# Performance work log

Hardware: AMD Instinct MI355X
Metric: run time of the kernel (lower is better)

## Reference

```python
import jax, jax.numpy as jnp
import numpy as np

# Static conv hyperparameters (match init_kwargs / setup_inputs)
PAD = 1
DIL = 1
STRIDE_VAL = 2.5          # continuous stride value used in setup_inputs
INT_STRIDE = 2            # floor(STRIDE_VAL): used for output-size arithmetic (static)


def _bilinear_take(x, pos, axis):
    """Linearly interpolate x along `axis` at fractional positions `pos`.

    pos has shape [O, K]; the sampled axis of x is replaced by the two axes
    (O, K). Out-of-range samples contribute zero (deform-conv convention).
    """
    n = x.shape[axis]
    p0 = jnp.floor(pos).astype(jnp.int32)
    frac = (pos - p0.astype(pos.dtype))
    out_shape = x.shape[:axis] + pos.shape + x.shape[axis + 1:]
    bshape = (1,) * axis + pos.shape + (1,) * (x.ndim - axis - 1)

    def take(p):
        valid = ((p >= 0) & (p < n)).astype(x.dtype).reshape(bshape)
        v = jnp.take(x, jnp.clip(p, 0, n - 1).reshape(-1), axis=axis)
        return v.reshape(out_shape) * valid

    w = frac.reshape(bshape).astype(x.dtype)
    return take(p0) * (1.0 - w) + take(p0 + 1) * w


def setup_inputs() -> dict:
    key = jax.random.key(0)
    k1, k2, k3 = jax.random.split(key, 3)
    x = jax.random.normal(k1, (32, 128, 64, 64), dtype=jnp.float32)
    weight = jax.random.normal(k2, (256, 128, 3, 3), dtype=jnp.float32) * 0.05
    bias = jax.random.normal(k3, (256,), dtype=jnp.float32)
    stride_h = jnp.full((1,), STRIDE_VAL, dtype=jnp.float32)
    stride_w = jnp.full((1,), STRIDE_VAL, dtype=jnp.float32)
    return {"x": x, "weight": weight, "bias": bias,
            "stride_h": stride_h, "stride_w": stride_w}


def reference(x, weight, bias, stride_h, stride_w):
    B, C, H, W = x.shape
    O, _, KH, KW = weight.shape
    # output size uses floor(stride), exactly as StrideConv2dFunction._output_size
    OH = (H + 2 * PAD - DIL * (KH - 1) - 1) // INT_STRIDE + 1
    OW = (W + 2 * PAD - DIL * (KW - 1) - 1) // INT_STRIDE + 1
    # fractional im2col sampling positions: out_idx * stride - pad + k * dilation
    pos_h = (jnp.arange(OH, dtype=jnp.float32)[:, None] * stride_h[0]
             - PAD + jnp.arange(KH, dtype=jnp.float32)[None, :] * DIL)  # [OH,KH]
    pos_w = (jnp.arange(OW, dtype=jnp.float32)[:, None] * stride_w[0]
             - PAD + jnp.arange(KW, dtype=jnp.float32)[None, :] * DIL)  # [OW,KW]
    rows = _bilinear_take(x, pos_h, axis=2)          # [B,C,OH,KH,W]
    patches = _bilinear_take(rows, pos_w, axis=4)    # [B,C,OH,KH,OW,KW]
    out = jnp.einsum('bcpkql,ockl->bopq', patches, weight)  # [B,O,OH,OW]
    return out + bias[None, :, None, None]
```

## Files before the change

### kernel.cpp

```cpp
#include <hip/hip_runtime.h>
#include <cstddef>

#define BB  32
#define CC  128
#define HH  64
#define WW  64
#define OO  256
#define OHH 32
#define OWW 32
#define YSTR 196
#define PSTR 296
#define ROWE (32 * YSTR)

typedef __bf16 bf16x8 __attribute__((ext_vector_type(8)));
typedef __bf16 bf16x4 __attribute__((ext_vector_type(4)));
typedef float  f32x4  __attribute__((ext_vector_type(4)));

__global__ void wtrans_bf16_kernel(const float* __restrict__ w, __bf16* __restrict__ wt) {
    int idx = blockIdx.x * 256 + threadIdx.x;
    if (idx >= OO * 9 * CC) return;
    int c    = idx & 127;
    int rest = idx >> 7;
    int k    = rest % 9;
    int o    = rest / 9;
    wt[idx] = (__bf16)w[((size_t)o * CC + c) * 9 + k];
}

__global__ __launch_bounds__(512, 2)
void conv_mfma_kernel(const float* __restrict__ x, const __bf16* __restrict__ wt,
                      const float* __restrict__ bias, const float* __restrict__ shp,
                      const float* __restrict__ swp, float* __restrict__ out) {
    __shared__ __align__(16) __bf16 yrbuf[4 + 4 * ROWE];
    __shared__ __align__(16) __bf16 pT[128 * PSTR];

    const int tid = threadIdx.x;
    const int b   = blockIdx.x;
    const int p0  = blockIdx.y * 4;
    const float sh = shp[0];
    const float sw = swp[0];

    float fh_[4];
    int   hb_[4];
    bool  oob[4];
#pragma unroll
    for (int pi = 0; pi < 4; ++pi) {
        float hpos = (float)(p0 + pi) * sh - 1.0f;
        float hbf  = floorf(hpos);
        fh_[pi] = hpos - hbf;
        hb_[pi] = (int)hbf;
        oob[pi] = (hb_[pi] >= HH || hb_[pi] <= -4);
    }

    if (oob[0] && oob[1] && oob[2] && oob[3]) {
#pragma unroll
        for (int j = 0; j < 16; ++j) {
            int fi = j * 512 + tid;
            int o  = fi >> 5;
            int rem = fi & 31;
            int pi = rem >> 3;
            int qf = rem & 7;
            float bv = bias[o];
            float4 r; r.x = bv; r.y = bv; r.z = bv; r.w = bv;
            *(float4*)(out + (((size_t)b * OO + o) * OHH + p0 + pi) * OWW + qf * 4) = r;
        }
        return;
    }

    const int piA = tid >> 7;
    const int t7  = tid & 127;
    const int cA  = t7 >> 2;
    const int cg0 = (t7 & 3) * 16;
    const float fhA = fh_[piA];
    int  hrA[4];
    bool rvA[4];
#pragma unroll
    for (int r = 0; r < 4; ++r) {
        hrA[r] = hb_[piA] + r;
        rvA[r] = (hrA[r] >= 0) && (hrA[r] < HH);
    }
    __bf16* yrA = yrbuf + 4 + piA * ROWE;

    const int piB = tid >> 7;
    const int qB  = (tid >> 2) & 31;
    const int cB  = (tid & 3) * 8;
    const float wposB = (float)qB * sw - 1.0f;
    const float wbfB  = floorf(wposB);
    const float fw    = wposB - wbfB;
    const int   wbq   = (int)wbfB;
    const int   wba   = min(wbq & ~3, 60);
    const int   e     = wbq - wba;
    const bool  g1 = e >= 1, g2 = e >= 2, g3 = e >= 3;
    bool mv[4];
#pragma unroll
    for (int j = 0; j < 4; ++j) mv[j] = ((unsigned)(wbq + j) < (unsigned)WW);
    const __bf16* yrB = yrbuf + 4 + piB * ROWE;
    __bf16* pqRow = pT + (piB * 32 + qB) * PSTR;

    const int wv = tid >> 6;
    const int l  = tid & 63;
    const int lr = l & 15;
    const int lg = l >> 4;
    const int o0 = wv * 32;

    f32x4 acc[2][8];
#pragma unroll
    for (int ot = 0; ot < 2; ++ot)
#pragma unroll
        for (int nt = 0; nt < 8; ++nt) acc[ot][nt] = (f32x4)0.0f;

    if (tid < 4) yrbuf[tid] = (__bf16)0.0f;

    for (int chunk = 0; chunk < 4; ++chunk) {
        const int c0 = chunk * 32;

        {
            const float* xp = x + ((size_t)(b * CC + c0 + cA) * HH) * WW;
            float4 v[4][4];
#pragma unroll
            for (int r = 0; r < 4; ++r) {
                if (rvA[r]) {
                    const float* rp = xp + (size_t)hrA[r] * WW + cg0;
#pragma unroll
                    for (int g = 0; g < 4; ++g) v[r][g] = *(const float4*)(rp + g * 4);
                } else {
#pragma unroll
                    for (int g = 0; g < 4; ++g) { v[r][g].x = 0.f; v[r][g].y = 0.f; v[r][g].z = 0.f; v[r][g].w = 0.f; }
                }
            }
            __bf16* yw = yrA + cA * YSTR + cg0;
#pragma unroll
            for (int kh = 0; kh < 3; ++kh) {
#pragma unroll
                for (int g = 0; g < 4; ++g) {
                    bf16x4 t;
                    t[0] = (__bf16)(v[kh][g].x + fhA * (v[kh + 1][g].x - v[kh][g].x));
                    t[1] = (__bf16)(v[kh][g].y + fhA * (v[kh + 1][g].y - v[kh][g].y));
                    t[2] = (__bf16)(v[kh][g].z + fhA * (v[kh + 1][g].z - v[kh][g].z));
                    t[3] = (__bf16)(v[kh][g].w + fhA * (v[kh + 1][g].w - v[kh][g].w));
                    *(bf16x4*)(yw + kh * 64 + g * 4) = t;
                }
            }
        }
        __syncthreads();

#pragma unroll
        for (int g = 0; g < 2; ++g) {
            const int cc0 = cB + g * 4;
            float tv[3][3][4];
#pragma unroll
            for (int ci = 0; ci < 4; ++ci) {
                const __bf16* yc = yrB + (cc0 + ci) * YSTR + wba;
#pragma unroll
                for (int kh = 0; kh < 3; ++kh) {
                    bf16x4 a  = *(const bf16x4*)(yc + kh * 64);
                    bf16x4 bq = *(const bf16x4*)(yc + kh * 64 + 4);
                    float v0 = (float)a[0], v1 = (float)a[1], v2 = (float)a[2], v3 = (float)a[3];
                    float v4 = (float)bq[0], v5 = (float)bq[1], v6 = (float)bq[2];
                    float s0 = g1 ? v1 : v0; s0 = g2 ? v2 : s0; s0 = g3 ? v3 : s0;
                    float s1 = g1 ? v2 : v1; s1 = g2 ? v3 : s1; s1 = g3 ? v4 : s1;
                    float s2 = g1 ? v3 : v2; s2 = g2 ? v4 : s2; s2 = g3 ? v5 : s2;
                    float s3 = g1 ? v4 : v3; s3 = g2 ? v5 : s3; s3 = g3 ? v6 : s3;
                    s0 = mv[0] ? s0 : 0.0f;
                    s1 = mv[1] ? s1 : 0.0f;
                    s2 = mv[2] ? s2 : 0.0f;
                    s3 = mv[3] ? s3 : 0.0f;
                    tv[kh][0][ci] = s0 + fw * (s1 - s0);
                    tv[kh][1][ci] = s1 + fw * (s2 - s1);
                    tv[kh][2][ci] = s2 + fw * (s3 - s2);
                }
            }
#pragma unroll
            for (int kh = 0; kh < 3; ++kh)
#pragma unroll
                for (int kw = 0; kw < 3; ++kw) {
                    bf16x4 pr;
                    pr[0] = (__bf16)tv[kh][kw][0];
                    pr[1] = (__bf16)tv[kh][kw][1];
                    pr[2] = (__bf16)tv[kh][kw][2];
                    pr[3] = (__bf16)tv[kh][kw][3];
                    *(bf16x4*)(pqRow + (kh * 3 + kw) * 32 + cc0) = pr;
                }
        }
        __syncthreads();

        __builtin_amdgcn_s_setprio(1);
#pragma unroll
        for (int k = 0; k < 9; ++k) {
            const __bf16* wp = wt + ((size_t)(o0 + lr) * 9 + k) * CC + c0 + lg * 8;
            bf16x8 a0 = *(const bf16x8*)(wp);
            bf16x8 a1 = *(const bf16x8*)(wp + (size_t)16 * 9 * CC);
            bf16x8 bfr[8];
#pragma unroll
            for (int nt = 0; nt < 8; ++nt)
                bfr[nt] = *(const bf16x8*)&pT[(nt * 16 + lr) * PSTR + k * 32 + lg * 8];
#pragma unroll
            for (int nt = 0; nt < 8; ++nt) {
                acc[0][nt] = __builtin_amdgcn_mfma_f32_16x16x32_bf16(a0, bfr[nt], acc[0][nt], 0, 0, 0);
                acc[1][nt] = __builtin_amdgcn_mfma_f32_16x16x32_bf16(a1, bfr[nt], acc[1][nt], 0, 0, 0);
            }
        }
        __builtin_amdgcn_s_setprio(0);
    }

#pragma unroll
    for (int ot = 0; ot < 2; ++ot) {
#pragma unroll
        for (int r = 0; r < 4; ++r) {
            int o = o0 + ot * 16 + lg * 4 + r;
            float bv = bias[o];
#pragma unroll
            for (int nt = 0; nt < 8; ++nt) {
                int pi = nt >> 1;
                int qc = (nt & 1) * 16 + lr;
                out[(((size_t)b * OO + o) * OHH + p0 + pi) * OWW + qc] = acc[ot][nt][r] + bv;
            }
        }
    }
}

__global__ __launch_bounds__(256)
void conv_fallback_kernel(const float* __restrict__ x, const float* __restrict__ w,
                          const float* __restrict__ bias, const float* __restrict__ shp,
                          const float* __restrict__ swp, float* __restrict__ out) {
    __shared__ __align__(16) float xr[4][WW];
    __shared__ __align__(16) float patch[9][OWW];
    const int tid = threadIdx.x;
    const int p = blockIdx.y;
    const int b = blockIdx.x;
    const float sh = shp[0];
    const float sw = swp[0];
    const float hpos = (float)p * sh - 1.0f;
    const float hbf  = floorf(hpos);
    const float fh   = hpos - hbf;
    const int   hb   = (int)hbf;
    const int og = tid & 63;
    const int qg = tid >> 6;
    const int o0 = og * 4;
    const int q0 = qg * 8;
    const int rr   = tid >> 6;
    const int colc = tid & 63;
    const int rowg = hb + rr;
    const bool rv = (rowg >= 0) && (rowg < HH);
    float acc[4][8];
#pragma unroll
    for (int i = 0; i < 4; ++i)
#pragma unroll
        for (int j = 0; j < 8; ++j) acc[i][j] = 0.0f;
    for (int c = 0; c < CC; ++c) {
        float vv = 0.0f;
        if (rv) vv = x[(((size_t)b * CC + c) * HH + rowg) * WW + colc];
        xr[rr][colc] = vv;
        __syncthreads();
        for (int it = tid; it < 9 * OWW; it += 256) {
            int k = it >> 5; int q = it & 31;
            int kh = k / 3;  int kw = k - kh * 3;
            float wpos = (float)q * sw - 1.0f + (float)kw;
            float wbf = floorf(wpos);
            float fw = wpos - wbf;
            int wb = (int)wbf;
            float x00 = 0, x01 = 0, x10 = 0, x11 = 0;
            if (wb >= 0 && wb < WW)         { x00 = xr[kh][wb];     x10 = xr[kh + 1][wb]; }
            if (wb + 1 >= 0 && wb + 1 < WW) { x01 = xr[kh][wb + 1]; x11 = xr[kh + 1][wb + 1]; }
            float top = x00 * (1.0f - fw) + x01 * fw;
            float bot = x10 * (1.0f - fw) + x11 * fw;
            patch[k][q] = top * (1.0f - fh) + bot * fh;
        }
        __syncthreads();
        const float4* pv = (const float4*)&patch[0][0];
#pragma unroll
        for (int k = 0; k < 9; ++k) {
            const float* wb_ = w + (size_t)o0 * (CC * 9) + c * 9 + k;
            float wvv[4] = {wb_[0], wb_[1 * CC * 9], wb_[2 * CC * 9], wb_[3 * CC * 9]};
            float4 pa = pv[k * 8 + (q0 >> 2)];
            float4 pb = pv[k * 8 + (q0 >> 2) + 1];
#pragma unroll
            for (int oo2 = 0; oo2 < 4; ++oo2) {
                acc[oo2][0] += wvv[oo2] * pa.x; acc[oo2][1] += wvv[oo2] * pa.y;
                acc[oo2][2] += wvv[oo2] * pa.z; acc[oo2][3] += wvv[oo2] * pa.w;
                acc[oo2][4] += wvv[oo2] * pb.x; acc[oo2][5] += wvv[oo2] * pb.y;
                acc[oo2][6] += wvv[oo2] * pb.z; acc[oo2][7] += wvv[oo2] * pb.w;
            }
        }
    }
    float4 bv = ((const float4*)bias)[og];
    float bvv[4] = {bv.x, bv.y, bv.z, bv.w};
#pragma unroll
    for (int oo2 = 0; oo2 < 4; ++oo2) {
        size_t off = (((size_t)b * OO + o0 + oo2) * OHH + p) * OWW + q0;
        float4 r0, r1;
        r0.x = acc[oo2][0] + bvv[oo2]; r0.y = acc[oo2][1] + bvv[oo2];
        r0.z = acc[oo2][2] + bvv[oo2]; r0.w = acc[oo2][3] + bvv[oo2];
        r1.x = acc[oo2][4] + bvv[oo2]; r1.y = acc[oo2][5] + bvv[oo2];
        r1.z = acc[oo2][6] + bvv[oo2]; r1.w = acc[oo2][7] + bvv[oo2];
        *(float4*)(out + off)     = r0;
        *(float4*)(out + off + 4) = r1;
    }
}

extern "C" void kernel_launch(void* const* d_in, const int* in_sizes, int n_in,
                              void* d_out, int out_size, void* d_ws, size_t ws_size,
                              hipStream_t stream) {
    const float* x    = (const float*)d_in[0];
    const float* w    = (const float*)d_in[1];
    const float* bias = (const float*)d_in[2];
    const float* shp  = (const float*)d_in[3];
    const float* swp  = (const float*)d_in[4];
    float* out = (float*)d_out;

    const size_t wt_bytes = (size_t)OO * 9 * CC * sizeof(__bf16);
    if (ws_size >= wt_bytes) {
        __bf16* wtp = (__bf16*)d_ws;
        int n = OO * 9 * CC;
        wtrans_bf16_kernel<<<(n + 255) / 256, 256, 0, stream>>>(w, wtp);
        dim3 grid(BB, OHH / 4);
        conv_mfma_kernel<<<grid, 512, 0, stream>>>(x, wtp, bias, shp, swp, out);
    } else {
        dim3 grid(BB, OHH);
        conv_fallback_kernel<<<grid, 256, 0, stream>>>(x, w, bias, shp, swp, out);
    }
}
```

Measured before the change: 55.08 us.

## Software-pipeline conv stages across half-tiles with double-buffered LDS and register-cached weights

The per-chunk loop is split into two half-tiles (row pairs), each with its own LDS buffers. Global loads for the next chunk, the horizontal interpolation of one half and the MFMA work on the other half are interleaved so loads and ALU overlap with matrix work across fewer barrier-separated phases. Weight fragments for a chunk are loaded once into registers and reused for both halves. The cost is higher register pressure (9x2 bf16x8 weight fragments plus pinned prefetch registers), which could cause spills or reduce occupancy at 512 threads with 2 blocks per CU.

```diff
diff --git a/kernel.cpp b/kernel.cpp
--- a/kernel.cpp
+++ b/kernel.cpp
@@ -9,8 +9,10 @@
 #define OHH 32
 #define OWW 32
 #define YSTR 196
+#define PROW (32 * YSTR)
+#define YRHALF (2 * PROW)
 #define PSTR 296
-#define ROWE (32 * YSTR)
+#define PTHALF (64 * PSTR)
 
 typedef __bf16 bf16x8 __attribute__((ext_vector_type(8)));
 typedef __bf16 bf16x4 __attribute__((ext_vector_type(4)));
@@ -30,8 +32,8 @@
 void conv_mfma_kernel(const float* __restrict__ x, const __bf16* __restrict__ wt,
                       const float* __restrict__ bias, const float* __restrict__ shp,
                       const float* __restrict__ swp, float* __restrict__ out) {
-    __shared__ __align__(16) __bf16 yrbuf[4 + 4 * ROWE];
-    __shared__ __align__(16) __bf16 pT[128 * PSTR];
+    __shared__ __align__(16) __bf16 yrbuf[8 + 2 * YRHALF + 8];
+    __shared__ __align__(16) __bf16 pT[2 * PTHALF];
 
     const int tid = threadIdx.x;
     const int b   = blockIdx.x;
@@ -66,23 +68,23 @@
         return;
     }
 
-    const int piA = tid >> 7;
-    const int t7  = tid & 127;
-    const int cA  = t7 >> 2;
-    const int cg0 = (t7 & 3) * 16;
-    const float fhA = fh_[piA];
-    int  hrA[4];
-    bool rvA[4];
-#pragma unroll
-    for (int r = 0; r < 4; ++r) {
-        hrA[r] = hb_[piA] + r;
-        rvA[r] = (hrA[r] >= 0) && (hrA[r] < HH);
-    }
-    __bf16* yrA = yrbuf + 4 + piA * ROWE;
-
-    const int piB = tid >> 7;
-    const int qB  = (tid >> 2) & 31;
-    const int cB  = (tid & 3) * 8;
+    const int pi2A = tid >> 8;
+    const int cA   = (tid >> 3) & 31;
+    const int colg = (tid & 7) * 8;
+    int  hr4[4][4];
+    bool rv4[4][4];
+#pragma unroll
+    for (int pi = 0; pi < 4; ++pi)
+#pragma unroll
+        for (int r = 0; r < 4; ++r) {
+            hr4[pi][r] = hb_[pi] + r;
+            rv4[pi][r] = (hr4[pi][r] >= 0) && (hr4[pi][r] < HH);
+        }
+
+    const int qB2  = tid >> 3;
+    const int pi2B = qB2 >> 5;
+    const int qB   = qB2 & 31;
+    const int cg0  = (tid & 7) * 4;
     const float wposB = (float)qB * sw - 1.0f;
     const float wbfB  = floorf(wposB);
     const float fw    = wposB - wbfB;
@@ -93,8 +95,6 @@
     bool mv[4];
 #pragma unroll
     for (int j = 0; j < 4; ++j) mv[j] = ((unsigned)(wbq + j) < (unsigned)WW);
-    const __bf16* yrB = yrbuf + 4 + piB * ROWE;
-    __bf16* pqRow = pT + (piB * 32 + qB) * PSTR;
 
     const int wv = tid >> 6;
     const int l  = tid & 63;
@@ -108,99 +108,140 @@
 #pragma unroll
         for (int nt = 0; nt < 8; ++nt) acc[ot][nt] = (f32x4)0.0f;
 
-    if (tid < 4) yrbuf[tid] = (__bf16)0.0f;
-
-    for (int chunk = 0; chunk < 4; ++chunk) {
-        const int c0 = chunk * 32;
-
-        {
-            const float* xp = x + ((size_t)(b * CC + c0 + cA) * HH) * WW;
-            float4 v[4][4];
-#pragma unroll
-            for (int r = 0; r < 4; ++r) {
-                if (rvA[r]) {
-                    const float* rp = xp + (size_t)hrA[r] * WW + cg0;
-#pragma unroll
-                    for (int g = 0; g < 4; ++g) v[r][g] = *(const float4*)(rp + g * 4);
-                } else {
-#pragma unroll
-                    for (int g = 0; g < 4; ++g) { v[r][g].x = 0.f; v[r][g].y = 0.f; v[r][g].z = 0.f; v[r][g].w = 0.f; }
-                }
-            }
-            __bf16* yw = yrA + cA * YSTR + cg0;
+    if (tid < 8) yrbuf[tid] = (__bf16)0.0f;
+
+    float4 vx[2][4];
+    bf16x8 wa[9][2];
+
+    auto aIssue = [&](int c0, int P) {
+        const int p = P * 2 + pi2A;
+        const float* xp = x + ((size_t)(b * CC + c0 + cA) * HH) * WW + colg;
+#pragma unroll
+        for (int r = 0; r < 4; ++r) {
+            float4 t0 = {0.f, 0.f, 0.f, 0.f}, t1 = t0;
+            if (rv4[p][r]) {
+                const float* rp = xp + (size_t)hr4[p][r] * WW;
+                t0 = *(const float4*)(rp);
+                t1 = *(const float4*)(rp + 4);
+            }
+            vx[0][r] = t0;
+            vx[1][r] = t1;
+        }
+    };
+
+    auto aFinish = [&](int P) {
+        const int p = P * 2 + pi2A;
+        const float fh = fh_[p];
+        __bf16* yw = yrbuf + 8 + P * YRHALF + pi2A * PROW + cA * YSTR + colg;
+#pragma unroll
+        for (int kh = 0; kh < 3; ++kh) {
+#pragma unroll
+            for (int h = 0; h < 2; ++h) {
+                float4 a = vx[h][kh], d = vx[h][kh + 1];
+                bf16x4 t;
+                t[0] = (__bf16)(a.x + fh * (d.x - a.x));
+                t[1] = (__bf16)(a.y + fh * (d.y - a.y));
+                t[2] = (__bf16)(a.z + fh * (d.z - a.z));
+                t[3] = (__bf16)(a.w + fh * (d.w - a.w));
+                *(bf16x4*)(yw + kh * 64 + h * 4) = t;
+            }
+        }
+    };
+
+    auto doB = [&](int P) {
+        const __bf16* ybase = yrbuf + 8 + P * YRHALF + pi2B * PROW;
+        __bf16* pq = pT + P * PTHALF + qB2 * PSTR;
+        float tv[3][3][4];
+#pragma unroll
+        for (int ci = 0; ci < 4; ++ci) {
+            const __bf16* yc = ybase + (cg0 + ci) * YSTR + wba;
 #pragma unroll
             for (int kh = 0; kh < 3; ++kh) {
-#pragma unroll
-                for (int g = 0; g < 4; ++g) {
-                    bf16x4 t;
-                    t[0] = (__bf16)(v[kh][g].x + fhA * (v[kh + 1][g].x - v[kh][g].x));
-                    t[1] = (__bf16)(v[kh][g].y + fhA * (v[kh + 1][g].y - v[kh][g].y));
-                    t[2] = (__bf16)(v[kh][g].z + fhA * (v[kh + 1][g].z - v[kh][g].z));
-                    t[3] = (__bf16)(v[kh][g].w + fhA * (v[kh + 1][g].w - v[kh][g].w));
-                    *(bf16x4*)(yw + kh * 64 + g * 4) = t;
-                }
-            }
-        }
+                bf16x4 a  = *(const bf16x4*)(yc + kh * 64);
+                bf16x4 bq = *(const bf16x4*)(yc + kh * 64 + 4);
+                float v0 = (float)a[0], v1 = (float)a[1], v2 = (float)a[2], v3 = (float)a[3];
+                float v4 = (float)bq[0], v5 = (float)bq[1], v6 = (float)bq[2];
+                float s0 = g1 ? v1 : v0; s0 = g2 ? v2 : s0; s0 = g3 ? v3 : s0;
+                float s1 = g1 ? v2 : v1; s1 = g2 ? v3 : s1; s1 = g3 ? v4 : s1;
+                float s2 = g1 ? v3 : v2; s2 = g2 ? v4 : s2; s2 = g3 ? v5 : s2;
+                float s3 = g1 ? v4 : v3; s3 = g2 ? v5 : s3; s3 = g3 ? v6 : s3;
+                s0 = mv[0] ? s0 : 0.0f;
+                s1 = mv[1] ? s1 : 0.0f;
+                s2 = mv[2] ? s2 : 0.0f;
+                s3 = mv[3] ? s3 : 0.0f;
+                tv[kh][0][ci] = s0 + fw * (s1 - s0);
+                tv[kh][1][ci] = s1 + fw * (s2 - s1);
+                tv[kh][2][ci] = s2 + fw * (s3 - s2);
+            }
+        }
+#pragma unroll
+        for (int kh = 0; kh < 3; ++kh)
+#pragma unroll
+            for (int kw = 0; kw < 3; ++kw) {
+                bf16x4 pr;
+                pr[0] = (__bf16)tv[kh][kw][0];
+                pr[1] = (__bf16)tv[kh][kw][1];
+                pr[2] = (__bf16)tv[kh][kw][2];
+                pr[3] = (__bf16)tv[kh][kw][3];
+                *(bf16x4*)(pq + (kh * 3 + kw) * 32 + cg0) = pr;
+            }
+    };
+
+    auto doM = [&](int c0, int nh, bool loadA) {
+        __builtin_amdgcn_s_setprio(1);
+#pragma unroll
+        for (int k = 0; k < 9; ++k) {
+            if (loadA) {
+                const __bf16* wp = wt + ((size_t)(o0 + lr) * 9 + k) * CC + c0 + lg * 8;
+                wa[k][0] = *(const bf16x8*)(wp);
+                wa[k][1] = *(const bf16x8*)(wp + (size_t)16 * 9 * CC);
+            }
+            const __bf16* pb = pT + nh * PTHALF + lr * PSTR + k * 32 + lg * 8;
+            bf16x8 b0 = *(const bf16x8*)(pb);
+            bf16x8 b1 = *(const bf16x8*)(pb + 16 * PSTR);
+            bf16x8 b2 = *(const bf16x8*)(pb + 32 * PSTR);
+            bf16x8 b3 = *(const bf16x8*)(pb + 48 * PSTR);
+            acc[0][nh * 4 + 0] = __builtin_amdgcn_mfma_f32_16x16x32_bf16(wa[k][0], b0, acc[0][nh * 4 + 0], 0, 0, 0);
+            acc[0][nh * 4 + 1] = __builtin_amdgcn_mfma_f32_16x16x32_bf16(wa[k][0], b1, acc[0][nh * 4 + 1], 0, 0, 0);
+            acc[0][nh * 4 + 2] = __builtin_amdgcn_mfma_f32_16x16x32_bf16(wa[k][0], b2, acc[0][nh * 4 + 2], 0, 0, 0);
+            acc[0][nh * 4 + 3] = __builtin_amdgcn_mfma_f32_16x16x32_bf16(wa[k][0], b3, acc[0][nh * 4 + 3], 0, 0, 0);
+            acc[1][nh * 4 + 0] = __builtin_amdgcn_mfma_f32_16x16x32_bf16(wa[k][1], b0, acc[1][nh * 4 + 0], 0, 0, 0);
+            acc[1][nh * 4 + 1] = __builtin_amdgcn_mfma_f32_16x16x32_bf16(wa[k][1], b1, acc[1][nh * 4 + 1], 0, 0, 0);
+            acc[1][nh * 4 + 2] = __builtin_amdgcn_mfma_f32_16x16x32_bf16(wa[k][1], b2, acc[1][nh * 4 + 2], 0, 0, 0);
+            acc[1][nh * 4 + 3] = __builtin_amdgcn_mfma_f32_16x16x32_bf16(wa[k][1], b3, acc[1][nh * 4 + 3], 0, 0, 0);
+        }
+        __builtin_amdgcn_s_setprio(0);
+    };
+
+#define PIN_VX() asm volatile("" :: \
+    "v"(vx[0][0].x), "v"(vx[0][1].x), "v"(vx[0][2].x), "v"(vx[0][3].x), \
+    "v"(vx[1][0].x), "v"(vx[1][1].x), "v"(vx[1][2].x), "v"(vx[1][3].x))
+
+    aIssue(0, 0); aFinish(0);
+    __syncthreads();
+    aIssue(0, 1); doB(0); aFinish(1);
+    __syncthreads();
+
+#pragma unroll
+    for (int c = 0; c < 3; ++c) {
+        aIssue((c + 1) * 32, 0);
+        doB(1);
+        PIN_VX();
+        doM(c * 32, 0, true);
+        aFinish(0);
         __syncthreads();
-
-#pragma unroll
-        for (int g = 0; g < 2; ++g) {
-            const int cc0 = cB + g * 4;
-            float tv[3][3][4];
-#pragma unroll
-            for (int ci = 0; ci < 4; ++ci) {
-                const __bf16* yc = yrB + (cc0 + ci) * YSTR + wba;
-#pragma unroll
-                for (int kh = 0; kh < 3; ++kh) {
-                    bf16x4 a  = *(const bf16x4*)(yc + kh * 64);
-                    bf16x4 bq = *(const bf16x4*)(yc + kh * 64 + 4);
-                    float v0 = (float)a[0], v1 = (float)a[1], v2 = (float)a[2], v3 = (float)a[3];
-                    float v4 = (float)bq[0], v5 = (float)bq[1], v6 = (float)bq[2];
-                    float s0 = g1 ? v1 : v0; s0 = g2 ? v2 : s0; s0 = g3 ? v3 : s0;
-                    float s1 = g1 ? v2 : v1; s1 = g2 ? v3 : s1; s1 = g3 ? v4 : s1;
-                    float s2 = g1 ? v3 : v2; s2 = g2 ? v4 : s2; s2 = g3 ? v5 : s2;
-                    float s3 = g1 ? v4 : v3; s3 = g2 ? v5 : s3; s3 = g3 ? v6 : s3;
-                    s0 = mv[0] ? s0 : 0.0f;
-                    s1 = mv[1] ? s1 : 0.0f;
-                    s2 = mv[2] ? s2 : 0.0f;
-                    s3 = mv[3] ? s3 : 0.0f;
-                    tv[kh][0][ci] = s0 + fw * (s1 - s0);
-                    tv[kh][1][ci] = s1 + fw * (s2 - s1);
-                    tv[kh][2][ci] = s2 + fw * (s3 - s2);
-                }
-            }
-#pragma unroll
-            for (int kh = 0; kh < 3; ++kh)
-#pragma unroll
-                for (int kw = 0; kw < 3; ++kw) {
-                    bf16x4 pr;
-                    pr[0] = (__bf16)tv[kh][kw][0];
-                    pr[1] = (__bf16)tv[kh][kw][1];
-                    pr[2] = (__bf16)tv[kh][kw][2];
-                    pr[3] = (__bf16)tv[kh][kw][3];
-                    *(bf16x4*)(pqRow + (kh * 3 + kw) * 32 + cc0) = pr;
-                }
-        }
+        aIssue((c + 1) * 32, 1);
+        doB(0);
+        PIN_VX();
+        doM(c * 32, 1, false);
+        aFinish(1);
         __syncthreads();
-
-        __builtin_amdgcn_s_setprio(1);
-#pragma unroll
-        for (int k = 0; k < 9; ++k) {
-            const __bf16* wp = wt + ((size_t)(o0 + lr) * 9 + k) * CC + c0 + lg * 8;
-            bf16x8 a0 = *(const bf16x8*)(wp);
-            bf16x8 a1 = *(const bf16x8*)(wp + (size_t)16 * 9 * CC);
-            bf16x8 bfr[8];
-#pragma unroll
-            for (int nt = 0; nt < 8; ++nt)
-                bfr[nt] = *(const bf16x8*)&pT[(nt * 16 + lr) * PSTR + k * 32 + lg * 8];
-#pragma unroll
-            for (int nt = 0; nt < 8; ++nt) {
-                acc[0][nt] = __builtin_amdgcn_mfma_f32_16x16x32_bf16(a0, bfr[nt], acc[0][nt], 0, 0, 0);
-                acc[1][nt] = __builtin_amdgcn_mfma_f32_16x16x32_bf16(a1, bfr[nt], acc[1][nt], 0, 0, 0);
-            }
-        }
-        __builtin_amdgcn_s_setprio(0);
-    }
+    }
+    doB(1);
+    doM(96, 0, true);
+    __syncthreads();
+    doM(96, 1, false);
+#undef PIN_VX
 
 #pragma unroll
     for (int ot = 0; ot < 2; ++ot) {
@@ -256,13 +297,13 @@
             int kh = k / 3;  int kw = k - kh * 3;
             float wpos = (float)q * sw - 1.0f + (float)kw;
             float wbf = floorf(wpos);
-            float fw = wpos - wbf;
+            float fwl = wpos - wbf;
             int wb = (int)wbf;
             float x00 = 0, x01 = 0, x10 = 0, x11 = 0;
             if (wb >= 0 && wb < WW)         { x00 = xr[kh][wb];     x10 = xr[kh + 1][wb]; }
             if (wb + 1 >= 0 && wb + 1 < WW) { x01 = xr[kh][wb + 1]; x11 = xr[kh + 1][wb + 1]; }
-            float top = x00 * (1.0f - fw) + x01 * fw;
-            float bot = x10 * (1.0f - fw) + x11 * fw;
+            float top = x00 * (1.0f - fwl) + x01 * fwl;
+            float bot = x10 * (1.0f - fwl) + x11 * fwl;
             patch[k][q] = top * (1.0f - fh) + bot * fh;
         }
         __syncthreads();
```

After: 56.14 us. Within noise of the previous version (+1.9%).

## Warp-specialize: half the waves run MFMA while others prefetch next channel chunk

Applied to the files above, without the earlier changes.

Waves 0-3 now compute all 256 output channels (64 each, four A fragments) while waves 4-7 load and row-interpolate the next 32-channel chunk of x into the shared row buffer. The first chunk is loaded before the loop. The aim is to overlap global loads and interpolation with the matrix-core work instead of running them back to back behind barriers. The cost is a doubled accumulator set (128 VGPRs), which may lower occupancy, and only half the waves issuing MFMAs.

```diff
diff --git a/kernel.cpp b/kernel.cpp
--- a/kernel.cpp
+++ b/kernel.cpp
@@ -79,6 +79,21 @@
         rvA[r] = (hrA[r] >= 0) && (hrA[r] < HH);
     }
     __bf16* yrA = yrbuf + 4 + piA * ROWE;
+
+    const int t8   = tid & 255;
+    const int piA2 = t8 >> 6;
+    const int u6   = t8 & 63;
+    const int cA2  = u6 >> 1;
+    const int colh = (u6 & 1) * 32;
+    const float fhA2 = fh_[piA2];
+    int  hrA2[4];
+    bool rvA2[4];
+#pragma unroll
+    for (int r = 0; r < 4; ++r) {
+        hrA2[r] = hb_[piA2] + r;
+        rvA2[r] = (hrA2[r] >= 0) && (hrA2[r] < HH);
+    }
+    __bf16* yrA2 = yrbuf + 4 + piA2 * ROWE;
 
     const int piB = tid >> 7;
     const int qB  = (tid >> 2) & 31;
@@ -100,48 +115,47 @@
     const int l  = tid & 63;
     const int lr = l & 15;
     const int lg = l >> 4;
-    const int o0 = wv * 32;
-
-    f32x4 acc[2][8];
-#pragma unroll
-    for (int ot = 0; ot < 2; ++ot)
+    const int o0 = (wv & 3) * 64;
+
+    f32x4 acc[4][8];
+#pragma unroll
+    for (int ot = 0; ot < 4; ++ot)
 #pragma unroll
         for (int nt = 0; nt < 8; ++nt) acc[ot][nt] = (f32x4)0.0f;
 
     if (tid < 4) yrbuf[tid] = (__bf16)0.0f;
+
+    {
+        const float* xp = x + ((size_t)(b * CC + cA) * HH) * WW;
+        float4 v[4][4];
+#pragma unroll
+        for (int r = 0; r < 4; ++r) {
+            if (rvA[r]) {
+                const float* rp = xp + (size_t)hrA[r] * WW + cg0;
+#pragma unroll
+                for (int g = 0; g < 4; ++g) v[r][g] = *(const float4*)(rp + g * 4);
+            } else {
+#pragma unroll
+                for (int g = 0; g < 4; ++g) { v[r][g].x = 0.f; v[r][g].y = 0.f; v[r][g].z = 0.f; v[r][g].w = 0.f; }
+            }
+        }
+        __bf16* yw = yrA + cA * YSTR + cg0;
+#pragma unroll
+        for (int kh = 0; kh < 3; ++kh)
+#pragma unroll
+            for (int g = 0; g < 4; ++g) {
+                bf16x4 t;
+                t[0] = (__bf16)(v[kh][g].x + fhA * (v[kh + 1][g].x - v[kh][g].x));
+                t[1] = (__bf16)(v[kh][g].y + fhA * (v[kh + 1][g].y - v[kh][g].y));
+                t[2] = (__bf16)(v[kh][g].z + fhA * (v[kh + 1][g].z - v[kh][g].z));
+                t[3] = (__bf16)(v[kh][g].w + fhA * (v[kh + 1][g].w - v[kh][g].w));
+                *(bf16x4*)(yw + kh * 64 + g * 4) = t;
+            }
+    }
+    __syncthreads();
 
     for (int chunk = 0; chunk < 4; ++chunk) {
         const int c0 = chunk * 32;
-
-        {
-            const float* xp = x + ((size_t)(b * CC + c0 + cA) * HH) * WW;
-            float4 v[4][4];
-#pragma unroll
-            for (int r = 0; r < 4; ++r) {
-                if (rvA[r]) {
-                    const float* rp = xp + (size_t)hrA[r] * WW + cg0;
-#pragma unroll
-                    for (int g = 0; g < 4; ++g) v[r][g] = *(const float4*)(rp + g * 4);
-                } else {
-#pragma unroll
-                    for (int g = 0; g < 4; ++g) { v[r][g].x = 0.f; v[r][g].y = 0.f; v[r][g].z = 0.f; v[r][g].w = 0.f; }
-                }
-            }
-            __bf16* yw = yrA + cA * YSTR + cg0;
-#pragma unroll
-            for (int kh = 0; kh < 3; ++kh) {
-#pragma unroll
-                for (int g = 0; g < 4; ++g) {
-                    bf16x4 t;
-                    t[0] = (__bf16)(v[kh][g].x + fhA * (v[kh + 1][g].x - v[kh][g].x));
-                    t[1] = (__bf16)(v[kh][g].y + fhA * (v[kh + 1][g].y - v[kh][g].y));
-                    t[2] = (__bf16)(v[kh][g].z + fhA * (v[kh + 1][g].z - v[kh][g].z));
-                    t[3] = (__bf16)(v[kh][g].w + fhA * (v[kh + 1][g].w - v[kh][g].w));
-                    *(bf16x4*)(yw + kh * 64 + g * 4) = t;
-                }
-            }
-        }
-        __syncthreads();
 
 #pragma unroll
         for (int g = 0; g < 2; ++g) {
@@ -183,36 +197,68 @@
         }
         __syncthreads();
 
-        __builtin_amdgcn_s_setprio(1);
-#pragma unroll
-        for (int k = 0; k < 9; ++k) {
-            const __bf16* wp = wt + ((size_t)(o0 + lr) * 9 + k) * CC + c0 + lg * 8;
-            bf16x8 a0 = *(const bf16x8*)(wp);
-            bf16x8 a1 = *(const bf16x8*)(wp + (size_t)16 * 9 * CC);
-            bf16x8 bfr[8];
-#pragma unroll
-            for (int nt = 0; nt < 8; ++nt)
-                bfr[nt] = *(const bf16x8*)&pT[(nt * 16 + lr) * PSTR + k * 32 + lg * 8];
-#pragma unroll
-            for (int nt = 0; nt < 8; ++nt) {
-                acc[0][nt] = __builtin_amdgcn_mfma_f32_16x16x32_bf16(a0, bfr[nt], acc[0][nt], 0, 0, 0);
-                acc[1][nt] = __builtin_amdgcn_mfma_f32_16x16x32_bf16(a1, bfr[nt], acc[1][nt], 0, 0, 0);
-            }
-        }
-        __builtin_amdgcn_s_setprio(0);
-    }
-
-#pragma unroll
-    for (int ot = 0; ot < 2; ++ot) {
-#pragma unroll
-        for (int r = 0; r < 4; ++r) {
-            int o = o0 + ot * 16 + lg * 4 + r;
-            float bv = bias[o];
-#pragma unroll
-            for (int nt = 0; nt < 8; ++nt) {
-                int pi = nt >> 1;
-                int qc = (nt & 1) * 16 + lr;
-                out[(((size_t)b * OO + o) * OHH + p0 + pi) * OWW + qc] = acc[ot][nt][r] + bv;
+        if (wv < 4) {
+            __builtin_amdgcn_s_setprio(1);
+#pragma unroll
+            for (int k = 0; k < 9; ++k) {
+                const __bf16* wp = wt + ((size_t)(o0 + lr) * 9 + k) * CC + c0 + lg * 8;
+                bf16x8 a0 = *(const bf16x8*)(wp);
+                bf16x8 a1 = *(const bf16x8*)(wp + (size_t)16 * 9 * CC);
+                bf16x8 a2 = *(const bf16x8*)(wp + (size_t)32 * 9 * CC);
+                bf16x8 a3 = *(const bf16x8*)(wp + (size_t)48 * 9 * CC);
+                bf16x8 bfr[8];
+#pragma unroll
+                for (int nt = 0; nt < 8; ++nt)
+                    bfr[nt] = *(const bf16x8*)&pT[(nt * 16 + lr) * PSTR + k * 32 + lg * 8];
+#pragma unroll
+                for (int nt = 0; nt < 8; ++nt) {
+                    acc[0][nt] = __builtin_amdgcn_mfma_f32_16x16x32_bf16(a0, bfr[nt], acc[0][nt], 0, 0, 0);
+                    acc[1][nt] = __builtin_amdgcn_mfma_f32_16x16x32_bf16(a1, bfr[nt], acc[1][nt], 0, 0, 0);
+                    acc[2][nt] = __builtin_amdgcn_mfma_f32_16x16x32_bf16(a2, bfr[nt], acc[2][nt], 0, 0, 0);
+                    acc[3][nt] = __builtin_amdgcn_mfma_f32_16x16x32_bf16(a3, bfr[nt], acc[3][nt], 0, 0, 0);
+                }
+            }
+            __builtin_amdgcn_s_setprio(0);
+        } else if (chunk < 3) {
+            const int c0n = c0 + 32;
+            const float* xp = x + ((size_t)(b * CC + c0n + cA2) * HH) * WW + colh;
+            __bf16* yw = yrA2 + cA2 * YSTR + colh;
+#pragma unroll
+            for (int g = 0; g < 8; ++g) {
+                float4 v[4];
+#pragma unroll
+                for (int r = 0; r < 4; ++r) {
+                    float4 t = {0.f, 0.f, 0.f, 0.f};
+                    if (rvA2[r]) t = *(const float4*)(xp + (size_t)hrA2[r] * WW + g * 4);
+                    v[r] = t;
+                }
+#pragma unroll
+                for (int kh = 0; kh < 3; ++kh) {
+                    bf16x4 t;
+                    t[0] = (__bf16)(v[kh].x + fhA2 * (v[kh + 1].x - v[kh].x));
+                    t[1] = (__bf16)(v[kh].y + fhA2 * (v[kh + 1].y - v[kh].y));
+                    t[2] = (__bf16)(v[kh].z + fhA2 * (v[kh + 1].z - v[kh].z));
+                    t[3] = (__bf16)(v[kh].w + fhA2 * (v[kh + 1].w - v[kh].w));
+                    *(bf16x4*)(yw + kh * 64 + g * 4) = t;
+                }
+            }
+        }
+        __syncthreads();
+    }
+
+    if (wv < 4) {
+#pragma unroll
+        for (int ot = 0; ot < 4; ++ot) {
+#pragma unroll
+            for (int r = 0; r < 4; ++r) {
+                int o = o0 + ot * 16 + lg * 4 + r;
+                float bv = bias[o];
+#pragma unroll
+                for (int nt = 0; nt < 8; ++nt) {
+                    int pi = nt >> 1;
+                    int qc = (nt & 1) * 16 + lr;
+                    out[(((size_t)b * OO + o) * OHH + p0 + pi) * OWW + qc] = acc[ot][nt][r] + bv;
+                }
             }
         }
     }
@@ -256,13 +302,13 @@
             int kh = k / 3;  int kw = k - kh * 3;
             float wpos = (float)q * sw - 1.0f + (float)kw;
             float wbf = floorf(wpos);
-            float fw = wpos - wbf;
+            float fwl = wpos - wbf;
             int wb = (int)wbf;
             float x00 = 0, x01 = 0, x10 = 0, x11 = 0;
             if (wb >= 0 && wb < WW)         { x00 = xr[kh][wb];     x10 = xr[kh + 1][wb]; }
             if (wb + 1 >= 0 && wb + 1 < WW) { x01 = xr[kh][wb + 1]; x11 = xr[kh + 1][wb + 1]; }
-            float top = x00 * (1.0f - fw) + x01 * fw;
-            float bot = x10 * (1.0f - fw) + x11 * fw;
+            float top = x00 * (1.0f - fwl) + x01 * fwl;
+            float bot = x10 * (1.0f - fwl) + x11 * fwl;
             patch[k][q] = top * (1.0f - fh) + bot * fh;
         }
         __syncthreads();
```

Result: slower. 65.53 us (+19.0%).
